# Kernel tuning notes

Measured on AMD Instinct MI355X. Metric: run time of the kernel, lower is better.

The kernel has to match this reference:

```python
import jax, jax.numpy as jnp
import numpy as np

N_EMBD = 1024
N_HEAD = 16
HEAD_SIZE = N_EMBD // N_HEAD  # 64


def rotate_half(x):
    x1, x2 = x[..., : x.shape[-1] // 2], x[..., x.shape[-1] // 2 :]
    return jnp.concatenate([-x2, x1], axis=-1)


def rope_cos_sin(T, head_size, dtype):
    inv_freq = 1.0 / (10000.0 ** (jnp.arange(0, head_size, 2, dtype=jnp.float32) / head_size))
    t = jnp.arange(T, dtype=jnp.float32)
    freqs = jnp.outer(t, inv_freq)  # (T, D/2)
    emb = jnp.concatenate([freqs, freqs], axis=-1)  # (T, D)
    return jnp.cos(emb).astype(dtype), jnp.sin(emb).astype(dtype)


def setup_inputs() -> dict:
    key = jax.random.key(0)
    k1, k2, k3, k4 = jax.random.split(key, 4)
    B, T, C = 4, 4096, N_EMBD
    scale = 1.0 / np.sqrt(C)
    return {
        "x": jax.random.normal(k1, (B, T, C), dtype=jnp.float32),
        "sigma0": jnp.zeros((B, N_HEAD, HEAD_SIZE, HEAD_SIZE), dtype=jnp.float32),
        "w_qkv": jax.random.normal(k2, (3 * C, C), dtype=jnp.float32) * scale,
        "w_proj": jax.random.normal(k3, (C, C), dtype=jnp.float32) * scale,
        "eta": jnp.ones((1,), dtype=jnp.float32) * 0.1,
    }


def reference(x, sigma0, w_qkv, w_proj, eta):
    B, T, C = x.shape
    H, D = N_HEAD, HEAD_SIZE
    qkv = x @ w_qkv.T  # (B,T,3C)
    q, k, v = jnp.split(qkv, 3, axis=-1)
    # (B,T,C) -> (B,H,T,D)
    q = q.reshape(B, T, H, D).transpose(0, 2, 1, 3)
    k = k.reshape(B, T, H, D).transpose(0, 2, 1, 3)
    v = v.reshape(B, T, H, D).transpose(0, 2, 1, 3)
    cos, sin = rope_cos_sin(T, D, x.dtype)  # (T,D) broadcast over (B,H,T,D)
    q = q * cos + rotate_half(q) * sin
    k = k * cos + rotate_half(k) * sin
    q = jax.nn.relu(q)
    k = jax.nn.relu(k)
    # sequential Hebbian fast-weight scan over time
    q_t = q.transpose(2, 0, 1, 3)  # (T,B,H,D)
    k_t = k.transpose(2, 0, 1, 3)
    v_t = v.transpose(2, 0, 1, 3)
    eta_s = eta[0]

    def step(sigma, qkv_step):
        qt, kt, vt = qkv_step  # each (B,H,D)
        out_t = jnp.einsum("bhd,bhde->bhe", qt, sigma)  # read BEFORE update
        sigma = sigma + eta_s * jnp.einsum("bhd,bhe->bhde", kt, vt)
        return sigma, out_t

    sigma_final, outs = jax.lax.scan(step, sigma0, (q_t, k_t, v_t))
    # outs: (T,B,H,D) -> (B,T,C)
    out = outs.transpose(1, 0, 2, 3).reshape(B, T, C)
    out = out @ w_proj.T
    return out, sigma_final
```

## Files before the change

kernel.cpp:

```cpp
#include <hip/hip_runtime.h>
#include <hip/hip_bf16.h>
#include <cstdint>
#include <cstddef>

#define B_   4
#define T_   4096
#define C_   1024
#define H_   16
#define NC_  64
#define M_   (B_*T_)
#define N3_  (3*C_)
#define NTK  16

typedef __attribute__((ext_vector_type(4))) float  f32x4;
typedef __attribute__((ext_vector_type(8))) __bf16 bf16x8;
typedef __attribute__((ext_vector_type(4))) __bf16 bf16x4;
typedef __attribute__((ext_vector_type(8))) unsigned short u16x8;

__device__ __forceinline__ void glds16(void* lds, const void* g) {
  __builtin_amdgcn_global_load_lds((const __attribute__((address_space(1))) void*)g,
                                   (__attribute__((address_space(3))) void*)lds,
                                   16, 0, 0);
}
#define MFMA_BF16 __builtin_amdgcn_mfma_f32_16x16x32_bf16

#define LDW 72
__device__ __forceinline__ int sw_off(int row, int s) {
  return row * LDW + ((s ^ ((row >> 3) & 7)) << 3);
}

__global__ __launch_bounds__(256) void cvt_f32_bf16(const float* __restrict__ in,
                                                    __bf16* __restrict__ out, int n4) {
  int i = blockIdx.x * 256 + threadIdx.x;
  if (i >= n4) return;
  float4 v = reinterpret_cast<const float4*>(in)[i];
  bf16x4 o;
  o[0] = (__bf16)v.x; o[1] = (__bf16)v.y; o[2] = (__bf16)v.z; o[3] = (__bf16)v.w;
  reinterpret_cast<bf16x4*>(out)[i] = o;
}

__global__ __launch_bounds__(256) void rope_tab(float2* __restrict__ tab) {
  int gid = blockIdx.x * 256 + threadIdx.x;
  int t = gid >> 5, dp = gid & 31;
  float invf = exp2f(-(float)dp * (13.287712379549449f / 32.0f));
  float ang = (float)t * invf;
  float s, c;
  sincosf(ang, &s, &c);
  tab[gid] = make_float2(c, s);
}

template<int FUSE, int NBN>
__global__ __launch_bounds__(512) void gemm_8ph(const __bf16* __restrict__ A,
                                                const __bf16* __restrict__ Bt,
                                                void* __restrict__ Cout,
                                                const float2* __restrict__ tab,
                                                int N) {
  __shared__ __bf16 sA[2][2][128 * 64];
  __shared__ __bf16 sB[2][2][128 * 64];
  const int tid  = threadIdx.x;
  const int lane = tid & 63;
  const int wave = tid >> 6;
  const int wm = wave >> 2, wn = wave & 3;
  const int nwg = NBN * 64, cpx = nwg / 8;
  const int wgid = (int)blockIdx.x;
  const int swzid = (wgid % 8) * cpx + wgid / 8;
  const int bn = swzid % NBN, bm = swzid / NBN;
  const int fr = lane & 15, kq = lane >> 4;
  const int fr7 = fr & 7;
  const int K = C_;

  const int r_loc = tid >> 3;
  const int sslot = (tid & 7) ^ (r_loc & 7);
  const __bf16* Ag = A  + (size_t)(bm * 256 + r_loc) * K + sslot * 8;
  const __bf16* Bg = Bt + (size_t)(bn * 256 + r_loc) * K + sslot * 8;
  const __bf16* AgH[2] = { Ag, Ag + (size_t)128 * K };
  const __bf16* BgH[2] = { Bg, Bg + (size_t)128 * K };

  f32x4 acc[8][4];
#pragma unroll
  for (int i = 0; i < 8; i++)
#pragma unroll
    for (int j = 0; j < 4; j++) acc[i][j] = (f32x4)0.0f;

#pragma unroll
  for (int h = 0; h < 2; ++h) {
    glds16((char*)sA[0][h] +    0 + tid * 16, AgH[h]);
    glds16((char*)sA[0][h] + 8192 + tid * 16, AgH[h] + (size_t)64 * K);
    glds16((char*)sB[0][h] +    0 + tid * 16, BgH[h]);
    glds16((char*)sB[0][h] + 8192 + tid * 16, BgH[h] + (size_t)64 * K);
  }

  bf16x8 af[4][2], bfr[4][2];
  const int bloc = (wn & 1) * 64;

  for (int t = 0; t < NTK; ++t) {
    const int d = t & 1, nb = d ^ 1;
    const bool dostage = (t + 1 < NTK);
    const int kb1 = (t + 1) * 64;
    const char* Abh = (const char*)sA[d][wm];
    const char* Bbh = (const char*)sB[d][wn >> 1];

    if (dostage) {
      glds16((char*)sA[nb][0] +    0 + tid * 16, AgH[0] + kb1);
      glds16((char*)sA[nb][0] + 8192 + tid * 16, AgH[0] + (size_t)64 * K + kb1);
      glds16((char*)sA[nb][1] +    0 + tid * 16, AgH[1] + kb1);
      glds16((char*)sA[nb][1] + 8192 + tid * 16, AgH[1] + (size_t)64 * K + kb1);
      asm volatile("s_waitcnt vmcnt(4)" ::: "memory");
    } else {
      asm volatile("s_waitcnt vmcnt(0)" ::: "memory");
    }
    __builtin_amdgcn_sched_barrier(0);
    __builtin_amdgcn_s_barrier();
#pragma unroll
    for (int i = 0; i < 4; ++i)
#pragma unroll
      for (int kk = 0; kk < 2; ++kk)
        af[i][kk] = *(const bf16x8*)(Abh + (i * 16 + fr) * 128 + (((kk << 2) | kq) ^ fr7) * 16);
#pragma unroll
    for (int j = 0; j < 2; ++j)
#pragma unroll
      for (int kk = 0; kk < 2; ++kk)
        bfr[j][kk] = *(const bf16x8*)(Bbh + (bloc + j * 16 + fr) * 128 + (((kk << 2) | kq) ^ fr7) * 16);
    asm volatile("s_waitcnt lgkmcnt(0)" ::: "memory");
    __builtin_amdgcn_sched_barrier(0);
    __builtin_amdgcn_s_setprio(1);
#pragma unroll
    for (int i = 0; i < 4; ++i)
#pragma unroll
      for (int j = 0; j < 2; ++j) {
        acc[i][j] = MFMA_BF16(af[i][0], bfr[j][0], acc[i][j], 0, 0, 0);
        acc[i][j] = MFMA_BF16(af[i][1], bfr[j][1], acc[i][j], 0, 0, 0);
      }
    __builtin_amdgcn_s_setprio(0);
    __builtin_amdgcn_s_barrier();

#pragma unroll
    for (int j = 0; j < 2; ++j)
#pragma unroll
      for (int kk = 0; kk < 2; ++kk)
        bfr[j + 2][kk] = *(const bf16x8*)(Bbh + (bloc + (j + 2) * 16 + fr) * 128 + (((kk << 2) | kq) ^ fr7) * 16);
    if (dostage) {
      glds16((char*)sB[nb][0] +    0 + tid * 16, BgH[0] + kb1);
      glds16((char*)sB[nb][0] + 8192 + tid * 16, BgH[0] + (size_t)64 * K + kb1);
      glds16((char*)sB[nb][1] +    0 + tid * 16, BgH[1] + kb1);
      glds16((char*)sB[nb][1] + 8192 + tid * 16, BgH[1] + (size_t)64 * K + kb1);
    }
    __builtin_amdgcn_s_barrier();
    asm volatile("s_waitcnt lgkmcnt(0)" ::: "memory");
    __builtin_amdgcn_sched_barrier(0);
    __builtin_amdgcn_s_setprio(1);
#pragma unroll
    for (int i = 0; i < 4; ++i)
#pragma unroll
      for (int j = 0; j < 2; ++j) {
        acc[i][j + 2] = MFMA_BF16(af[i][0], bfr[j + 2][0], acc[i][j + 2], 0, 0, 0);
        acc[i][j + 2] = MFMA_BF16(af[i][1], bfr[j + 2][1], acc[i][j + 2], 0, 0, 0);
      }
    __builtin_amdgcn_s_setprio(0);
    __builtin_amdgcn_s_barrier();

#pragma unroll
    for (int i = 0; i < 4; ++i)
#pragma unroll
      for (int kk = 0; kk < 2; ++kk)
        af[i][kk] = *(const bf16x8*)(Abh + (64 + i * 16 + fr) * 128 + (((kk << 2) | kq) ^ fr7) * 16);
    asm volatile("s_waitcnt lgkmcnt(0)" ::: "memory");
    __builtin_amdgcn_sched_barrier(0);
    __builtin_amdgcn_s_setprio(1);
#pragma unroll
    for (int i = 0; i < 4; ++i)
#pragma unroll
      for (int j = 0; j < 2; ++j) {
        acc[i + 4][j] = MFMA_BF16(af[i][0], bfr[j][0], acc[i + 4][j], 0, 0, 0);
        acc[i + 4][j] = MFMA_BF16(af[i][1], bfr[j][1], acc[i + 4][j], 0, 0, 0);
      }
    __builtin_amdgcn_s_setprio(0);

    __builtin_amdgcn_s_setprio(1);
#pragma unroll
    for (int i = 0; i < 4; ++i)
#pragma unroll
      for (int j = 0; j < 2; ++j) {
        acc[i + 4][j + 2] = MFMA_BF16(af[i][0], bfr[j + 2][0], acc[i + 4][j + 2], 0, 0, 0);
        acc[i + 4][j + 2] = MFMA_BF16(af[i][1], bfr[j + 2][1], acc[i + 4][j + 2], 0, 0, 0);
      }
    __builtin_amdgcn_s_setprio(0);
    __builtin_amdgcn_s_barrier();
  }

  const int rg4 = kq * 4;
  const int cb = bn * 256 + wn * 64;
  if (FUSE == 1 && bn < 8) {
#pragma unroll
    for (int i = 0; i < 8; ++i)
#pragma unroll
      for (int r = 0; r < 4; ++r) {
        size_t row = (size_t)bm * 256 + wm * 128 + i * 16 + rg4 + r;
        int tt = (int)(row & (T_ - 1));
#pragma unroll
        for (int j = 0; j < 2; ++j) {
          int dp = j * 16 + fr;
          float2 cs = tab[tt * 32 + dp];
          float x1 = acc[i][j][r], x2 = acc[i][j + 2][r];
          float o1 = fmaxf(x1 * cs.x - x2 * cs.y, 0.0f);
          float o2 = fmaxf(x2 * cs.x + x1 * cs.y, 0.0f);
          ((__bf16*)Cout)[row * N + cb + j * 16 + fr]      = (__bf16)o1;
          ((__bf16*)Cout)[row * N + cb + j * 16 + fr + 32] = (__bf16)o2;
        }
      }
  } else {
#pragma unroll
    for (int i = 0; i < 8; ++i)
#pragma unroll
      for (int j = 0; j < 4; ++j) {
        size_t row = (size_t)bm * 256 + wm * 128 + i * 16 + rg4;
        size_t col = (size_t)cb + j * 16 + fr;
#pragma unroll
        for (int r = 0; r < 4; ++r) {
          if (FUSE == 2) ((float*)Cout)[(row + r) * N + col]  = acc[i][j][r];
          else           ((__bf16*)Cout)[(row + r) * N + col] = (__bf16)acc[i][j][r];
        }
      }
  }
}

__global__ __launch_bounds__(256) void chunk_kv(const __bf16* __restrict__ qkv,
                                                __bf16* __restrict__ G) {
  __shared__ __bf16 Kt[64 * LDW];
  __shared__ __bf16 Vt[64 * LDW];
  const int bid = blockIdx.x;
  const int c = bid & (NC_ - 1);
  const int bh = bid >> 6;
  const int h = bh & (H_ - 1);
  const int b = bh >> 4;
  const int tid = threadIdx.x;
  const size_t row0 = (size_t)b * T_ + c * 64;
  const int kcol = C_ + h * 64;
  const int vcol = 2 * C_ + h * 64;
#pragma unroll
  for (int it = 0; it < 2; ++it) {
    int task = tid + it * 256;
    int t = task >> 3;
    int d0 = (task & 7) * 8;
    const size_t rb = (row0 + t) * N3_;
    u16x8 kv = *(const u16x8*)(qkv + rb + kcol + d0);
    u16x8 vv = *(const u16x8*)(qkv + rb + vcol + d0);
    const int ts = t >> 3, tl = t & 7;
#pragma unroll
    for (int j = 0; j < 8; j++) {
      int d = d0 + j;
      ((unsigned short*)Kt)[sw_off(d, ts) + tl] = kv[j];
      ((unsigned short*)Vt)[sw_off(d, ts) + tl] = vv[j];
    }
  }
  __syncthreads();
  const int lane = tid & 63, wave = tid >> 6;
  const int gr = (wave >> 1) * 32, gc = (wave & 1) * 32;
  const int fr = lane & 15, kq = lane >> 4;
  f32x4 acc[2][2];
#pragma unroll
  for (int i = 0; i < 2; i++)
#pragma unroll
    for (int j = 0; j < 2; j++) acc[i][j] = (f32x4)0.0f;
#pragma unroll
  for (int kk = 0; kk < 2; ++kk) {
    bf16x8 af[2], bfr[2];
#pragma unroll
    for (int i = 0; i < 2; i++) {
      int row = gr + i * 16 + fr;
      af[i] = *(const bf16x8*)(Kt + sw_off(row, kk * 4 + kq));
    }
#pragma unroll
    for (int j = 0; j < 2; j++) {
      int row = gc + j * 16 + fr;
      bfr[j] = *(const bf16x8*)(Vt + sw_off(row, kk * 4 + kq));
    }
#pragma unroll
    for (int i = 0; i < 2; i++)
#pragma unroll
      for (int j = 0; j < 2; j++)
        acc[i][j] = MFMA_BF16(af[i], bfr[j], acc[i][j], 0, 0, 0);
  }
  const int rg = kq * 4;
  __bf16* Gb = G + (size_t)bid * 4096;
#pragma unroll
  for (int i = 0; i < 2; i++)
#pragma unroll
    for (int j = 0; j < 2; j++)
#pragma unroll
      for (int r = 0; r < 4; r++)
        Gb[(gr + i * 16 + rg + r) * 64 + gc + j * 16 + fr] = (__bf16)acc[i][j][r];
}

__global__ __launch_bounds__(256) void prefix_scan(const __bf16* __restrict__ G,
                                                   const float* __restrict__ sigma0,
                                                   __bf16* __restrict__ S,
                                                   float* __restrict__ sigma_out,
                                                   const float* __restrict__ eta) {
  const int blk = blockIdx.x;
  const int bh = blk >> 2;
  const int dq = blk & 3;
  const int tid = threadIdx.x;
  const int d = dq * 16 + (tid >> 4);
  const int e0 = (tid & 15) * 4;
  const float eta_s = eta[0];
  const size_t base_de = (size_t)d * 64 + e0;
  float acc[4], s0[4];
#pragma unroll
  for (int j = 0; j < 4; j++) {
    acc[j] = 0.0f;
    s0[j] = sigma0[(size_t)bh * 4096 + base_de + j];
  }
  for (int c = 0; c < NC_; ++c) {
    const size_t off = ((size_t)bh * NC_ + c) * 4096 + base_de;
    bf16x4 sv;
#pragma unroll
    for (int j = 0; j < 4; j++) sv[j] = (__bf16)(s0[j] + eta_s * acc[j]);
    *(bf16x4*)(S + off) = sv;
    bf16x4 g = *(const bf16x4*)(G + off);
#pragma unroll
    for (int j = 0; j < 4; j++) acc[j] += (float)g[j];
  }
  float4 v;
  v.x = s0[0] + eta_s * acc[0];
  v.y = s0[1] + eta_s * acc[1];
  v.z = s0[2] + eta_s * acc[2];
  v.w = s0[3] + eta_s * acc[3];
  *reinterpret_cast<float4*>(sigma_out + (size_t)bh * 4096 + base_de) = v;
}

__global__ __launch_bounds__(256) void chunk_out(const __bf16* __restrict__ qkv,
                                                 const __bf16* __restrict__ S,
                                                 __bf16* __restrict__ outp,
                                                 const float* __restrict__ eta) {
  __shared__ __bf16 Qs[64 * LDW];
  __shared__ __bf16 Ks[64 * LDW];
  __shared__ __bf16 Vt[64 * LDW];
  __shared__ __bf16 St[64 * LDW];
  __shared__ __bf16 Ps[64 * LDW];
  const int bid = blockIdx.x;
  const int c = bid & 63, bh = bid >> 6, h = bh & 15, b = bh >> 4;
  const int tid = threadIdx.x;
  const size_t row0 = (size_t)b * T_ + c * 64;
  const float eta_s = eta[0];
#pragma unroll
  for (int it = 0; it < 2; ++it) {
    int task = tid + it * 256;
    int t = task >> 3, d0 = (task & 7) * 8;
    const size_t rb = (row0 + t) * N3_;
    const int ds = d0 >> 3, ts = t >> 3, tl = t & 7;
    *(u16x8*)(Qs + sw_off(t, ds)) = *(const u16x8*)(qkv + rb + h * 64 + d0);
    *(u16x8*)(Ks + sw_off(t, ds)) = *(const u16x8*)(qkv + rb + C_ + h * 64 + d0);
    u16x8 vv = *(const u16x8*)(qkv + rb + 2 * C_ + h * 64 + d0);
    u16x8 sv = *(const u16x8*)(S + (size_t)bid * 4096 + t * 64 + d0);
#pragma unroll
    for (int j = 0; j < 8; j++) {
      int e = d0 + j;
      ((unsigned short*)Vt)[sw_off(e, ts) + tl] = vv[j];
      ((unsigned short*)St)[sw_off(e, ts) + tl] = sv[j];
    }
  }
  __syncthreads();
  const int lane = tid & 63, wave = tid >> 6;
  const int qr = (wave >> 1) * 32, qc = (wave & 1) * 32;
  const int fr = lane & 15, kq = lane >> 4, rg = (lane >> 4) * 4;
  {
    f32x4 pacc[2][2];
#pragma unroll
    for (int i = 0; i < 2; i++)
#pragma unroll
      for (int j = 0; j < 2; j++) pacc[i][j] = (f32x4)0.0f;
#pragma unroll
    for (int kk = 0; kk < 2; ++kk) {
      bf16x8 af[2], bfr[2];
#pragma unroll
      for (int i = 0; i < 2; i++) {
        int row = qr + i * 16 + fr;
        af[i] = *(const bf16x8*)(Qs + sw_off(row, kk * 4 + kq));
      }
#pragma unroll
      for (int j = 0; j < 2; j++) {
        int row = qc + j * 16 + fr;
        bfr[j] = *(const bf16x8*)(Ks + sw_off(row, kk * 4 + kq));
      }
#pragma unroll
      for (int i = 0; i < 2; i++)
#pragma unroll
        for (int j = 0; j < 2; j++)
          pacc[i][j] = MFMA_BF16(af[i], bfr[j], pacc[i][j], 0, 0, 0);
    }
#pragma unroll
    for (int i = 0; i < 2; i++)
#pragma unroll
      for (int j = 0; j < 2; j++)
#pragma unroll
        for (int r = 0; r < 4; r++) {
          int trow = qr + i * 16 + rg + r;
          int scol = qc + j * 16 + fr;
          float v = (scol < trow) ? eta_s * pacc[i][j][r] : 0.0f;
          Ps[sw_off(trow, scol >> 3) + (scol & 7)] = (__bf16)v;
        }
  }
  __syncthreads();
  {
    f32x4 oacc[2][2];
#pragma unroll
    for (int i = 0; i < 2; i++)
#pragma unroll
      for (int j = 0; j < 2; j++) oacc[i][j] = (f32x4)0.0f;
#pragma unroll
    for (int kk = 0; kk < 2; ++kk) {
      bf16x8 pa[2], vb[2], qa[2], sb[2];
#pragma unroll
      for (int i = 0; i < 2; i++) {
        int row = qr + i * 16 + fr;
        pa[i] = *(const bf16x8*)(Ps + sw_off(row, kk * 4 + kq));
        qa[i] = *(const bf16x8*)(Qs + sw_off(row, kk * 4 + kq));
      }
#pragma unroll
      for (int j = 0; j < 2; j++) {
        int row = qc + j * 16 + fr;
        vb[j] = *(const bf16x8*)(Vt + sw_off(row, kk * 4 + kq));
        sb[j] = *(const bf16x8*)(St + sw_off(row, kk * 4 + kq));
      }
#pragma unroll
      for (int i = 0; i < 2; i++)
#pragma unroll
        for (int j = 0; j < 2; j++) {
          oacc[i][j] = MFMA_BF16(pa[i], vb[j], oacc[i][j], 0, 0, 0);
          oacc[i][j] = MFMA_BF16(qa[i], sb[j], oacc[i][j], 0, 0, 0);
        }
    }
#pragma unroll
    for (int i = 0; i < 2; i++)
#pragma unroll
      for (int j = 0; j < 2; j++)
#pragma unroll
        for (int r = 0; r < 4; r++) {
          size_t row = row0 + qr + i * 16 + rg + r;
          int col = h * 64 + qc + j * 16 + fr;
          outp[row * C_ + col] = (__bf16)oacc[i][j][r];
        }
  }
}

extern "C" void kernel_launch(void* const* d_in, const int* in_sizes, int n_in,
                              void* d_out, int out_size, void* d_ws, size_t ws_size,
                              hipStream_t stream) {
  const float* x      = (const float*)d_in[0];
  const float* sigma0 = (const float*)d_in[1];
  const float* w_qkv  = (const float*)d_in[2];
  const float* w_proj = (const float*)d_in[3];
  const float* eta    = (const float*)d_in[4];
  float* out       = (float*)d_out;
  float* sigma_out = out + (size_t)M_ * C_;

  char* ws = (char*)d_ws;
  __bf16* xbf     = (__bf16*)(ws);
  __bf16* wqkvbf  = (__bf16*)(ws + 33554432);
  __bf16* wprojbf = (__bf16*)(ws + 39845888);
  __bf16* qkvbf   = (__bf16*)(ws + 41943040);
  __bf16* Gws     = (__bf16*)(ws + 142606336);
  __bf16* Sws     = (__bf16*)(ws + 176160768);
  float2* tab     = (float2*)(ws + 176160768);

  rope_tab<<<512, 256, 0, stream>>>(tab);
  cvt_f32_bf16<<<16384, 256, 0, stream>>>(x, xbf, 4194304);
  cvt_f32_bf16<<<3072, 256, 0, stream>>>(w_qkv, wqkvbf, 786432);
  cvt_f32_bf16<<<1024, 256, 0, stream>>>(w_proj, wprojbf, 262144);
  gemm_8ph<1, 12><<<768, 512, 0, stream>>>(xbf, wqkvbf, (void*)qkvbf, tab, N3_);
  chunk_kv<<<4096, 256, 0, stream>>>(qkvbf, Gws);
  prefix_scan<<<256, 256, 0, stream>>>(Gws, sigma0, Sws, sigma_out, eta);
  chunk_out<<<4096, 256, 0, stream>>>(qkvbf, Sws, xbf, eta);
  gemm_8ph<2, 4><<<256, 512, 0, stream>>>(xbf, wprojbf, (void*)out, nullptr, C_);
}
```

Before: 263.1 us.

## Replace 8-phase 256x256 GEMM with simpler 256x128 K32 double-buffered GEMM

Rewrites the bf16 GEMM from a 512-thread, 256x256-tile, K=64 eight-phase schedule into a 256-thread, 256x128-tile, K=32 kernel with one LDS-load phase and one MFMA burst per K step. The swizzled LDS layout now packs two rows per 128-byte line, and launch grids double in block count. The aim is more workgroups per CU and a simpler schedule. The cost is less reuse per tile, more barriers per K, and less overlap between loads and MFMAs.

```diff
diff --git a/kernel.cpp b/kernel.cpp
--- a/kernel.cpp
+++ b/kernel.cpp
@@ -10,7 +10,7 @@
 #define NC_  64
 #define M_   (B_*T_)
 #define N3_  (3*C_)
-#define NTK  16
+#define NT32 32
 
 typedef __attribute__((ext_vector_type(4))) float  f32x4;
 typedef __attribute__((ext_vector_type(8))) __bf16 bf16x8;
@@ -50,31 +50,29 @@
 }
 
 template<int FUSE, int NBN>
-__global__ __launch_bounds__(512) void gemm_8ph(const __bf16* __restrict__ A,
+__global__ __launch_bounds__(256) void gemm_s32(const __bf16* __restrict__ A,
                                                 const __bf16* __restrict__ Bt,
                                                 void* __restrict__ Cout,
                                                 const float2* __restrict__ tab,
                                                 int N) {
-  __shared__ __bf16 sA[2][2][128 * 64];
-  __shared__ __bf16 sB[2][2][128 * 64];
+  __shared__ __bf16 sA[2][256 * 32];
+  __shared__ __bf16 sB[2][128 * 32];
   const int tid  = threadIdx.x;
   const int lane = tid & 63;
   const int wave = tid >> 6;
-  const int wm = wave >> 2, wn = wave & 3;
+  const int wm = wave >> 1, wn = wave & 1;
   const int nwg = NBN * 64, cpx = nwg / 8;
   const int wgid = (int)blockIdx.x;
   const int swzid = (wgid % 8) * cpx + wgid / 8;
   const int bn = swzid % NBN, bm = swzid / NBN;
   const int fr = lane & 15, kq = lane >> 4;
-  const int fr7 = fr & 7;
   const int K = C_;
 
-  const int r_loc = tid >> 3;
-  const int sslot = (tid & 7) ^ (r_loc & 7);
-  const __bf16* Ag = A  + (size_t)(bm * 256 + r_loc) * K + sslot * 8;
-  const __bf16* Bg = Bt + (size_t)(bn * 256 + r_loc) * K + sslot * 8;
-  const __bf16* AgH[2] = { Ag, Ag + (size_t)128 * K };
-  const __bf16* BgH[2] = { Bg, Bg + (size_t)128 * K };
+  const int ssl = (tid & 7) ^ ((tid >> 3) & 7);
+  const int rloc = 2 * (tid >> 3) + (ssl >> 2);
+  const int kloc = (ssl & 3) * 8;
+  const __bf16* Ag = A  + (size_t)(bm * 256 + rloc) * K + kloc;
+  const __bf16* Bg = Bt + (size_t)(bn * 128 + rloc) * K + kloc;
 
   f32x4 acc[8][4];
 #pragma unroll
@@ -83,114 +81,64 @@
     for (int j = 0; j < 4; j++) acc[i][j] = (f32x4)0.0f;
 
 #pragma unroll
-  for (int h = 0; h < 2; ++h) {
-    glds16((char*)sA[0][h] +    0 + tid * 16, AgH[h]);
-    glds16((char*)sA[0][h] + 8192 + tid * 16, AgH[h] + (size_t)64 * K);
-    glds16((char*)sB[0][h] +    0 + tid * 16, BgH[h]);
-    glds16((char*)sB[0][h] + 8192 + tid * 16, BgH[h] + (size_t)64 * K);
-  }
-
-  bf16x8 af[4][2], bfr[4][2];
-  const int bloc = (wn & 1) * 64;
-
-  for (int t = 0; t < NTK; ++t) {
+  for (int q = 0; q < 4; ++q)
+    glds16((char*)sA[0] + q * 4096 + tid * 16, Ag + (size_t)q * 64 * K);
+#pragma unroll
+  for (int q = 0; q < 2; ++q)
+    glds16((char*)sB[0] + q * 4096 + tid * 16, Bg + (size_t)q * 64 * K);
+  asm volatile("s_waitcnt vmcnt(0)" ::: "memory");
+  __builtin_amdgcn_sched_barrier(0);
+  __builtin_amdgcn_s_barrier();
+
+  bf16x8 af[8], bfr[4];
+  for (int t = 0; t < NT32; ++t) {
     const int d = t & 1, nb = d ^ 1;
-    const bool dostage = (t + 1 < NTK);
-    const int kb1 = (t + 1) * 64;
-    const char* Abh = (const char*)sA[d][wm];
-    const char* Bbh = (const char*)sB[d][wn >> 1];
+    const bool dostage = (t + 1 < NT32);
+    const int kb1 = (t + 1) * 32;
+    const char* Ab = (const char*)sA[d];
+    const char* Bb = (const char*)sB[d];
 
     if (dostage) {
-      glds16((char*)sA[nb][0] +    0 + tid * 16, AgH[0] + kb1);
-      glds16((char*)sA[nb][0] + 8192 + tid * 16, AgH[0] + (size_t)64 * K + kb1);
-      glds16((char*)sA[nb][1] +    0 + tid * 16, AgH[1] + kb1);
-      glds16((char*)sA[nb][1] + 8192 + tid * 16, AgH[1] + (size_t)64 * K + kb1);
-      asm volatile("s_waitcnt vmcnt(4)" ::: "memory");
+#pragma unroll
+      for (int q = 0; q < 4; ++q)
+        glds16((char*)sA[nb] + q * 4096 + tid * 16, Ag + (size_t)q * 64 * K + kb1);
+#pragma unroll
+      for (int q = 0; q < 2; ++q)
+        glds16((char*)sB[nb] + q * 4096 + tid * 16, Bg + (size_t)q * 64 * K + kb1);
+      asm volatile("s_waitcnt vmcnt(6)" ::: "memory");
     } else {
       asm volatile("s_waitcnt vmcnt(0)" ::: "memory");
     }
     __builtin_amdgcn_sched_barrier(0);
     __builtin_amdgcn_s_barrier();
-#pragma unroll
-    for (int i = 0; i < 4; ++i)
-#pragma unroll
-      for (int kk = 0; kk < 2; ++kk)
-        af[i][kk] = *(const bf16x8*)(Abh + (i * 16 + fr) * 128 + (((kk << 2) | kq) ^ fr7) * 16);
-#pragma unroll
-    for (int j = 0; j < 2; ++j)
-#pragma unroll
-      for (int kk = 0; kk < 2; ++kk)
-        bfr[j][kk] = *(const bf16x8*)(Bbh + (bloc + j * 16 + fr) * 128 + (((kk << 2) | kq) ^ fr7) * 16);
+
+#pragma unroll
+    for (int i = 0; i < 8; ++i) {
+      int row = wm * 128 + i * 16 + fr;
+      int sr = row >> 1;
+      af[i] = *(const bf16x8*)(Ab + sr * 128 + ((((row & 1) << 2) | kq) ^ (sr & 7)) * 16);
+    }
+#pragma unroll
+    for (int j = 0; j < 4; ++j) {
+      int row = wn * 64 + j * 16 + fr;
+      int sr = row >> 1;
+      bfr[j] = *(const bf16x8*)(Bb + sr * 128 + ((((row & 1) << 2) | kq) ^ (sr & 7)) * 16);
+    }
     asm volatile("s_waitcnt lgkmcnt(0)" ::: "memory");
     __builtin_amdgcn_sched_barrier(0);
     __builtin_amdgcn_s_setprio(1);
 #pragma unroll
-    for (int i = 0; i < 4; ++i)
-#pragma unroll
-      for (int j = 0; j < 2; ++j) {
-        acc[i][j] = MFMA_BF16(af[i][0], bfr[j][0], acc[i][j], 0, 0, 0);
-        acc[i][j] = MFMA_BF16(af[i][1], bfr[j][1], acc[i][j], 0, 0, 0);
-      }
+    for (int i = 0; i < 8; ++i)
+#pragma unroll
+      for (int j = 0; j < 4; ++j)
+        acc[i][j] = MFMA_BF16(af[i], bfr[j], acc[i][j], 0, 0, 0);
     __builtin_amdgcn_s_setprio(0);
     __builtin_amdgcn_s_barrier();
-
-#pragma unroll
-    for (int j = 0; j < 2; ++j)
-#pragma unroll
-      for (int kk = 0; kk < 2; ++kk)
-        bfr[j + 2][kk] = *(const bf16x8*)(Bbh + (bloc + (j + 2) * 16 + fr) * 128 + (((kk << 2) | kq) ^ fr7) * 16);
-    if (dostage) {
-      glds16((char*)sB[nb][0] +    0 + tid * 16, BgH[0] + kb1);
-      glds16((char*)sB[nb][0] + 8192 + tid * 16, BgH[0] + (size_t)64 * K + kb1);
-      glds16((char*)sB[nb][1] +    0 + tid * 16, BgH[1] + kb1);
-      glds16((char*)sB[nb][1] + 8192 + tid * 16, BgH[1] + (size_t)64 * K + kb1);
-    }
-    __builtin_amdgcn_s_barrier();
-    asm volatile("s_waitcnt lgkmcnt(0)" ::: "memory");
-    __builtin_amdgcn_sched_barrier(0);
-    __builtin_amdgcn_s_setprio(1);
-#pragma unroll
-    for (int i = 0; i < 4; ++i)
-#pragma unroll
-      for (int j = 0; j < 2; ++j) {
-        acc[i][j + 2] = MFMA_BF16(af[i][0], bfr[j + 2][0], acc[i][j + 2], 0, 0, 0);
-        acc[i][j + 2] = MFMA_BF16(af[i][1], bfr[j + 2][1], acc[i][j + 2], 0, 0, 0);
-      }
-    __builtin_amdgcn_s_setprio(0);
-    __builtin_amdgcn_s_barrier();
-
-#pragma unroll
-    for (int i = 0; i < 4; ++i)
-#pragma unroll
-      for (int kk = 0; kk < 2; ++kk)
-        af[i][kk] = *(const bf16x8*)(Abh + (64 + i * 16 + fr) * 128 + (((kk << 2) | kq) ^ fr7) * 16);
-    asm volatile("s_waitcnt lgkmcnt(0)" ::: "memory");
-    __builtin_amdgcn_sched_barrier(0);
-    __builtin_amdgcn_s_setprio(1);
-#pragma unroll
-    for (int i = 0; i < 4; ++i)
-#pragma unroll
-      for (int j = 0; j < 2; ++j) {
-        acc[i + 4][j] = MFMA_BF16(af[i][0], bfr[j][0], acc[i + 4][j], 0, 0, 0);
-        acc[i + 4][j] = MFMA_BF16(af[i][1], bfr[j][1], acc[i + 4][j], 0, 0, 0);
-      }
-    __builtin_amdgcn_s_setprio(0);
-
-    __builtin_amdgcn_s_setprio(1);
-#pragma unroll
-    for (int i = 0; i < 4; ++i)
-#pragma unroll
-      for (int j = 0; j < 2; ++j) {
-        acc[i + 4][j + 2] = MFMA_BF16(af[i][0], bfr[j + 2][0], acc[i + 4][j + 2], 0, 0, 0);
-        acc[i + 4][j + 2] = MFMA_BF16(af[i][1], bfr[j + 2][1], acc[i + 4][j + 2], 0, 0, 0);
-      }
-    __builtin_amdgcn_s_setprio(0);
-    __builtin_amdgcn_s_barrier();
   }
 
   const int rg4 = kq * 4;
-  const int cb = bn * 256 + wn * 64;
-  if (FUSE == 1 && bn < 8) {
+  const int cb = bn * 128 + wn * 64;
+  if (FUSE == 1 && bn < 16) {
 #pragma unroll
     for (int i = 0; i < 8; ++i)
 #pragma unroll
@@ -468,9 +416,9 @@
   cvt_f32_bf16<<<16384, 256, 0, stream>>>(x, xbf, 4194304);
   cvt_f32_bf16<<<3072, 256, 0, stream>>>(w_qkv, wqkvbf, 786432);
   cvt_f32_bf16<<<1024, 256, 0, stream>>>(w_proj, wprojbf, 262144);
-  gemm_8ph<1, 12><<<768, 512, 0, stream>>>(xbf, wqkvbf, (void*)qkvbf, tab, N3_);
+  gemm_s32<1, 24><<<1536, 256, 0, stream>>>(xbf, wqkvbf, (void*)qkvbf, tab, N3_);
   chunk_kv<<<4096, 256, 0, stream>>>(qkvbf, Gws);
   prefix_scan<<<256, 256, 0, stream>>>(Gws, sigma0, Sws, sigma_out, eta);
   chunk_out<<<4096, 256, 0, stream>>>(qkvbf, Sws, xbf, eta);
-  gemm_8ph<2, 4><<<256, 512, 0, stream>>>(xbf, wprojbf, (void*)out, nullptr, C_);
-}
+  gemm_s32<2, 8><<<512, 256, 0, stream>>>(xbf, wprojbf, (void*)out, nullptr, C_);
+}
```

Result: slower. 384.5 us (+46.1%).
